# Optimization experiments

Hardware: AMD Instinct MI355X
Metric: run time of the kernel (lower is better)

Reference implementation:

```python
import jax, jax.numpy as jnp
import numpy as np

BETA = 0.95
THRESH = 1.0

def conv(x, w, b, stride):
    y = jax.lax.conv_general_dilated(x, w, (stride, stride), 'VALID',
                                     dimension_numbers=('NCHW', 'OIHW', 'NCHW'))
    return y + b[None, :, None, None]

def lif(mem, inp):
    # snntorch Leaky, reset_mechanism='subtract':
    # reset computed from previous mem, then mem = beta*mem + input - reset*thr, spk = H(mem - thr)
    reset = (mem > THRESH).astype(inp.dtype)
    mem = BETA * mem + inp - reset * THRESH
    spk = (mem > THRESH).astype(inp.dtype)
    return spk, mem

def setup_inputs() -> dict:
    key = jax.random.key(0)
    ks = jax.random.split(key, 7)
    B, T = 512, 4
    x = jax.random.uniform(ks[0], (B, T, 84, 84), jnp.float32) * 255.0  # raw pixel frames

    def init_conv(k, o, i, kh):
        lim = 1.0 / np.sqrt(i * kh * kh)
        k1, k2 = jax.random.split(k)
        return (jax.random.uniform(k1, (o, i, kh, kh), jnp.float32, -lim, lim),
                jax.random.uniform(k2, (o,), jnp.float32, -lim, lim))

    def init_lin(k, i, o):
        lim = 1.0 / np.sqrt(i)
        k1, k2 = jax.random.split(k)
        return (jax.random.uniform(k1, (o, i), jnp.float32, -lim, lim),
                jax.random.uniform(k2, (o,), jnp.float32, -lim, lim))

    w1, b1 = init_conv(ks[1], 32, 1, 8)
    w2, b2 = init_conv(ks[2], 64, 32, 4)
    w3, b3 = init_conv(ks[3], 64, 64, 3)
    wl, bl = init_lin(ks[4], 3136, 512)
    wh, bh = init_lin(ks[5], 512, 18)
    return {"x": x, "w1": w1, "b1": b1, "w2": w2, "b2": b2, "w3": w3, "b3": b3,
            "wl": wl, "bl": bl, "wh": wh, "bh": bh}

def reference(x, w1, b1, w2, b2, w3, b3, wl, bl, wh, bh):
    x = x / 255.0                                  # Plastic.forward scaling
    B, T = x.shape[0], x.shape[1]
    xt = jnp.transpose(x, (1, 0, 2, 3))[:, :, None]  # [T, B, 1, 84, 84]
    mem1 = jnp.zeros((B, 32, 20, 20), x.dtype)
    mem2 = jnp.zeros((B, 64, 9, 9), x.dtype)
    mem3 = jnp.zeros((B, 64, 7, 7), x.dtype)
    memf = jnp.zeros((B, 512), x.dtype)
    acc0 = jnp.zeros((B, 512), x.dtype)

    def step(carry, xs):
        mem1, mem2, mem3, memf, acc = carry
        o = conv(xs, w1, b1, 4)          # [B,32,20,20]
        s1, mem1 = lif(mem1, o)
        o = conv(s1, w2, b2, 2)          # [B,64,9,9]
        s2, mem2 = lif(mem2, o)
        o = conv(s2, w3, b3, 1)          # [B,64,7,7]
        s3, mem3 = lif(mem3, o)
        o = s3.reshape(B, -1) @ wl.T + bl  # [B,512]
        sf, memf = lif(memf, o)
        return (mem1, mem2, mem3, memf, acc + sf), None

    (mem1, mem2, mem3, memf, spk_out), _ = jax.lax.scan(
        step, (mem1, mem2, mem3, memf, acc0), xt)
    return (spk_out / T) @ wh.T + bh     # [B, 18]
```

## Files before the change

kernel.cpp:

```cpp
#include <hip/hip_runtime.h>

#define BETA 0.95f

__device__ __forceinline__ void lif_store(float inp, float* __restrict__ mem,
                                          float* __restrict__ spk, size_t idx, int t) {
    float m = t ? mem[idx] : 0.0f;
    float r = (m > 1.0f) ? 1.0f : 0.0f;
    m = BETA * m + inp - r;
    mem[idx] = m;
    spk[idx] = (m > 1.0f) ? 1.0f : 0.0f;
}

__global__ void transpose_w23(const float* __restrict__ w2, const float* __restrict__ w3,
                              float* __restrict__ w2t, float* __restrict__ w3t) {
    int i = blockIdx.x * 256 + threadIdx.x;
    if (i < 32768) { int oc = i >> 9;  int k = i & 511;      w2t[k * 64 + oc] = w2[i]; }
    if (i < 36864) { int oc = i / 576; int k = i - oc * 576; w3t[k * 64 + oc] = w3[i]; }
}

__global__ __launch_bounds__(320) void conv1_lif(const float* __restrict__ x,
        const float* __restrict__ w1, const float* __restrict__ b1,
        float* __restrict__ mem1, float* __restrict__ s1, int t)
{
    __shared__ float xs[7056];
    __shared__ __align__(16) float wt[2048];
    __shared__ float bs[32];
    const int b = blockIdx.x, tid = threadIdx.x;
    const float* xp = x + (size_t)(b * 4 + t) * 7056;
    for (int i = tid; i < 7056; i += 320) xs[i] = xp[i] * (1.0f / 255.0f);
    for (int i = tid; i < 2048; i += 320) { int oc = i >> 6, k = i & 63; wt[k * 32 + oc] = w1[i]; }
    if (tid < 32) bs[tid] = b1[tid];
    __syncthreads();

    const int ocg = tid & 7, row = tid >> 3;
    const int oc0 = ocg * 4;
    const int oy = row >> 1, ox0 = (row & 1) * 10;

    float acc[4][10];
    #pragma unroll
    for (int j = 0; j < 4; j++) {
        const float bv = bs[oc0 + j];
        #pragma unroll
        for (int i = 0; i < 10; i++) acc[j][i] = bv;
    }

    for (int ky = 0; ky < 8; ky++) {
        const float* xr = &xs[(oy * 4 + ky) * 84 + ox0 * 4];
        #pragma unroll
        for (int kx = 0; kx < 8; kx++) {
            const float4 w4 = *(const float4*)&wt[(ky * 8 + kx) * 32 + oc0];
            const float wv[4] = {w4.x, w4.y, w4.z, w4.w};
            float xv[10];
            #pragma unroll
            for (int i = 0; i < 10; i++) xv[i] = xr[kx + 4 * i];
            #pragma unroll
            for (int j = 0; j < 4; j++)
                #pragma unroll
                for (int i = 0; i < 10; i++)
                    acc[j][i] += wv[j] * xv[i];
        }
    }

    const size_t base = (size_t)b * 12800 + (size_t)oc0 * 400 + oy * 20 + ox0;
    #pragma unroll
    for (int j = 0; j < 4; j++)
        #pragma unroll
        for (int i = 0; i < 10; i++)
            lif_store(acc[j][i], mem1, s1, base + (size_t)j * 400 + i, t);
}

__global__ __launch_bounds__(448) void conv2_lif(const float* __restrict__ s1,
        const float* __restrict__ w2t, const float* __restrict__ b2,
        float* __restrict__ mem2, float* __restrict__ s2, int t)
{
    __shared__ float ins[12800];
    __shared__ __align__(16) float wt[64 * 64];
    __shared__ float bs[64];
    const int b = blockIdx.x, tid = threadIdx.x;
    const float* ip = s1 + (size_t)b * 12800;
    for (int i = tid; i < 12800; i += 448) ins[i] = ip[i];
    if (tid < 64) bs[tid] = b2[tid];

    const int ocg = tid & 15, pid = tid >> 4;
    const int oc0 = ocg * 4;
    const int oy = pid / 3, ox0 = (pid % 3) * 3;
    const bool act = (pid < 27);
    __syncthreads();

    float acc[4][3];
    #pragma unroll
    for (int j = 0; j < 4; j++) {
        const float bv = bs[oc0 + j];
        #pragma unroll
        for (int i = 0; i < 3; i++) acc[j][i] = bv;
    }

    for (int kc = 0; kc < 512; kc += 64) {
        for (int i = tid; i < 4096; i += 448) wt[i] = w2t[kc * 64 + i];
        __syncthreads();
        if (act) {
            const int ic0 = kc >> 4;
            #pragma unroll
            for (int icl = 0; icl < 4; icl++) {
                const float* inc = &ins[(ic0 + icl) * 400];
                #pragma unroll
                for (int ky = 0; ky < 4; ky++) {
                    const float* xr = &inc[(oy * 2 + ky) * 20 + ox0 * 2];
                    #pragma unroll
                    for (int kx = 0; kx < 4; kx++) {
                        const float4 w4 = *(const float4*)&wt[(icl * 16 + ky * 4 + kx) * 64 + oc0];
                        const float x0 = xr[kx], x1 = xr[kx + 2], x2 = xr[kx + 4];
                        acc[0][0] += w4.x * x0; acc[0][1] += w4.x * x1; acc[0][2] += w4.x * x2;
                        acc[1][0] += w4.y * x0; acc[1][1] += w4.y * x1; acc[1][2] += w4.y * x2;
                        acc[2][0] += w4.z * x0; acc[2][1] += w4.z * x1; acc[2][2] += w4.z * x2;
                        acc[3][0] += w4.w * x0; acc[3][1] += w4.w * x1; acc[3][2] += w4.w * x2;
                    }
                }
            }
        }
        __syncthreads();
    }

    if (act) {
        const size_t base = (size_t)b * 5184 + (size_t)oc0 * 81 + oy * 9 + ox0;
        #pragma unroll
        for (int j = 0; j < 4; j++)
            #pragma unroll
            for (int i = 0; i < 3; i++)
                lif_store(acc[j][i], mem2, s2, base + (size_t)j * 81 + i, t);
    }
}

__global__ __launch_bounds__(256) void conv3_lif(const float* __restrict__ s2,
        const float* __restrict__ w3t, const float* __restrict__ b3,
        float* __restrict__ mem3, float* __restrict__ s3, int t)
{
    __shared__ float ins[5184];
    __shared__ __align__(8) float wt[72 * 64];
    __shared__ float bs[64];
    const int b = blockIdx.x, tid = threadIdx.x;
    const float* ip = s2 + (size_t)b * 5184;
    for (int i = tid; i < 5184; i += 256) ins[i] = ip[i];
    if (tid < 64) bs[tid] = b3[tid];

    const int ocg = tid & 31, oy = tid >> 5;
    const int oc0 = ocg * 2;
    const bool act = (oy < 7);
    __syncthreads();

    float acc[2][7];
    #pragma unroll
    for (int j = 0; j < 2; j++) {
        const float bv = bs[oc0 + j];
        #pragma unroll
        for (int i = 0; i < 7; i++) acc[j][i] = bv;
    }

    for (int kc = 0; kc < 576; kc += 72) {
        for (int i = tid; i < 4608; i += 256) wt[i] = w3t[kc * 64 + i];
        __syncthreads();
        if (act) {
            const int ic0 = kc / 9;
            #pragma unroll
            for (int icl = 0; icl < 8; icl++) {
                const float* inc = &ins[(ic0 + icl) * 81];
                #pragma unroll
                for (int ky = 0; ky < 3; ky++) {
                    const float* xr = &inc[(oy + ky) * 9];
                    float xv[9];
                    #pragma unroll
                    for (int i = 0; i < 9; i++) xv[i] = xr[i];
                    #pragma unroll
                    for (int kx = 0; kx < 3; kx++) {
                        const float2 w2v = *(const float2*)&wt[(icl * 9 + ky * 3 + kx) * 64 + oc0];
                        #pragma unroll
                        for (int i = 0; i < 7; i++) {
                            acc[0][i] += w2v.x * xv[kx + i];
                            acc[1][i] += w2v.y * xv[kx + i];
                        }
                    }
                }
            }
        }
        __syncthreads();
    }

    if (act) {
        const size_t base = (size_t)b * 3136 + (size_t)oc0 * 49 + oy * 7;
        #pragma unroll
        for (int j = 0; j < 2; j++)
            #pragma unroll
            for (int i = 0; i < 7; i++)
                lif_store(acc[j][i], mem3, s3, base + (size_t)j * 49 + i, t);
    }
}

__global__ __launch_bounds__(256) void transpose_mk(const float* __restrict__ s3,
        const float* __restrict__ wl, float* __restrict__ s3t, float* __restrict__ wlt)
{
    __shared__ float T[64][65];
    const int c0 = blockIdx.x * 64;
    const int r0 = blockIdx.y * 64;
    const float* src = blockIdx.z ? wl : s3;
    float* dst = blockIdx.z ? wlt : s3t;
    const int tid = threadIdx.x;
    #pragma unroll
    for (int i = 0; i < 4; i++) {
        const int f = tid + 256 * i;
        const int r = f >> 4, cq = (f & 15) * 4;
        const float4 v = *(const float4*)&src[(size_t)(r0 + r) * 3136 + c0 + cq];
        T[r][cq + 0] = v.x; T[r][cq + 1] = v.y; T[r][cq + 2] = v.z; T[r][cq + 3] = v.w;
    }
    __syncthreads();
    #pragma unroll
    for (int i = 0; i < 4; i++) {
        const int f = tid + 256 * i;
        const int c = f >> 4, rq = (f & 15) * 4;
        float4 v;
        v.x = T[rq + 0][c]; v.y = T[rq + 1][c]; v.z = T[rq + 2][c]; v.w = T[rq + 3][c];
        *(float4*)&dst[(size_t)(c0 + c) * 512 + r0 + rq] = v;
    }
}

__global__ __launch_bounds__(256) void fc_gemm(const float* __restrict__ s3t,
        const float* __restrict__ wlt, float* __restrict__ part)
{
    __shared__ __align__(16) float As[64][68];
    __shared__ __align__(16) float Bs[64][68];
    const int bid = blockIdx.x;
    const int tile = bid & 63, split = bid >> 6;
    const int m0 = (tile & 7) * 64, n0 = (tile >> 3) * 64;
    const int tid = threadIdx.x;
    const int tn = (tid & 15) * 4, tm = (tid >> 4) * 4;
    float acc[4][4] = {};

    for (int sc = 0; sc < 7; sc++) {
        const int kc = split * 448 + sc * 64;
        __syncthreads();
        #pragma unroll
        for (int i = 0; i < 4; i++) {
            const int f = tid + 256 * i;
            const int k = f >> 4, mq = (f & 15) * 4;
            *(float4*)&As[k][mq] = *(const float4*)&s3t[(size_t)(kc + k) * 512 + m0 + mq];
            *(float4*)&Bs[k][mq] = *(const float4*)&wlt[(size_t)(kc + k) * 512 + n0 + mq];
        }
        __syncthreads();
        #pragma unroll 8
        for (int k = 0; k < 64; k++) {
            const float4 a = *(const float4*)&As[k][tm];
            const float4 b = *(const float4*)&Bs[k][tn];
            acc[0][0] += a.x * b.x; acc[0][1] += a.x * b.y; acc[0][2] += a.x * b.z; acc[0][3] += a.x * b.w;
            acc[1][0] += a.y * b.x; acc[1][1] += a.y * b.y; acc[1][2] += a.y * b.z; acc[1][3] += a.y * b.w;
            acc[2][0] += a.z * b.x; acc[2][1] += a.z * b.y; acc[2][2] += a.z * b.z; acc[2][3] += a.z * b.w;
            acc[3][0] += a.w * b.x; acc[3][1] += a.w * b.y; acc[3][2] += a.w * b.z; acc[3][3] += a.w * b.w;
        }
    }

    #pragma unroll
    for (int r = 0; r < 4; r++) {
        float4 v; v.x = acc[r][0]; v.y = acc[r][1]; v.z = acc[r][2]; v.w = acc[r][3];
        *(float4*)&part[(size_t)split * 262144 + (size_t)(m0 + tm + r) * 512 + n0 + tn] = v;
    }
}

__global__ __launch_bounds__(256) void fc_reduce_lif(const float* __restrict__ part,
        const float* __restrict__ bl, float* __restrict__ memf,
        float* __restrict__ accum, int t)
{
    const int gid = blockIdx.x * 256 + threadIdx.x;
    const int n = gid & 511;
    float s = part[gid];
    #pragma unroll
    for (int sp = 1; sp < 7; sp++) s += part[(size_t)sp * 262144 + gid];
    s += bl[n];
    const float mp = t ? memf[gid] : 0.0f;
    const float r = (mp > 1.0f) ? 1.0f : 0.0f;
    const float mnew = BETA * mp + s - r;
    memf[gid] = mnew;
    const float spk = (mnew > 1.0f) ? 1.0f : 0.0f;
    accum[gid] = (t ? accum[gid] : 0.0f) + spk;
}

__global__ void head_k(const float* __restrict__ accum, const float* __restrict__ wh,
                       const float* __restrict__ bh, float* __restrict__ out)
{
    const int gid = blockIdx.x * 256 + threadIdx.x;
    if (gid >= 512 * 18) return;
    const int b = gid / 18, o = gid - b * 18;
    const float* av = accum + (size_t)b * 512;
    const float* wv = wh + (size_t)o * 512;
    float s = bh[o];
    for (int k = 0; k < 512; k++) s += (av[k] * 0.25f) * wv[k];
    out[gid] = s;
}

extern "C" void kernel_launch(void* const* d_in, const int* in_sizes, int n_in,
                              void* d_out, int out_size, void* d_ws, size_t ws_size,
                              hipStream_t stream)
{
    const float* x  = (const float*)d_in[0];
    const float* w1 = (const float*)d_in[1];
    const float* b1 = (const float*)d_in[2];
    const float* w2 = (const float*)d_in[3];
    const float* b2 = (const float*)d_in[4];
    const float* w3 = (const float*)d_in[5];
    const float* b3 = (const float*)d_in[6];
    const float* wl = (const float*)d_in[7];
    const float* bl = (const float*)d_in[8];
    const float* wh = (const float*)d_in[9];
    const float* bh = (const float*)d_in[10];

    float* ws   = (float*)d_ws;
    float* mem1 = ws;
    float* mem2 = mem1 + 6553600;
    float* mem3 = mem2 + 2654208;
    float* memf = mem3 + 1605632;
    float* acc  = memf + 262144;
    float* s1   = acc  + 262144;
    float* s2   = s1 + 6553600;
    float* s3   = s2 + 2654208;
    float* w2t  = s3 + 1605632;
    float* w3t  = w2t + 32768;

    float* s3t_buf = s1;
    float* wlt_buf = s1 + 1605632;
    float* part    = s1 + 3211264;

    transpose_w23<<<144, 256, 0, stream>>>(w2, w3, w2t, w3t);

    for (int t = 0; t < 4; t++) {
        conv1_lif<<<512, 320, 0, stream>>>(x, w1, b1, mem1, s1, t);
        conv2_lif<<<512, 448, 0, stream>>>(s1, w2t, b2, mem2, s2, t);
        conv3_lif<<<512, 256, 0, stream>>>(s2, w3t, b3, mem3, s3, t);
        transpose_mk<<<dim3(49, 8, 2), 256, 0, stream>>>(s3, wl, s3t_buf, wlt_buf);
        fc_gemm<<<448, 256, 0, stream>>>(s3t_buf, wlt_buf, part);
        fc_reduce_lif<<<1024, 256, 0, stream>>>(part, bl, memf, acc, t);
    }
    head_k<<<36, 256, 0, stream>>>(acc, wh, bh, (float*)d_out);
}
```

Baseline: 1.107 ms.

## Retile conv2 so each thread computes a full output row for four channels

conv2 now uses 192 threads where each active thread computes 4 output channels by 9 output columns, in place of 4 by 3, and loads the input row as float4 vectors into registers. Input and weight staging into shared memory use float4 copies, and the barrier is moved to the top of the chunk loop. The aim is more reuse of each weight and input load per FMA and fewer idle threads. It raises register pressure (36 accumulators plus a 20-float row) and gives 48 of 192 threads nothing to compute, which may reduce occupancy.

```diff
diff --git a/kernel.cpp b/kernel.cpp
--- a/kernel.cpp
+++ b/kernel.cpp
@@ -69,35 +69,45 @@
             lif_store(acc[j][i], mem1, s1, base + (size_t)j * 400 + i, t);
 }
 
-__global__ __launch_bounds__(448) void conv2_lif(const float* __restrict__ s1,
+__global__ __launch_bounds__(192) void conv2_lif(const float* __restrict__ s1,
         const float* __restrict__ w2t, const float* __restrict__ b2,
         float* __restrict__ mem2, float* __restrict__ s2, int t)
 {
-    __shared__ float ins[12800];
-    __shared__ __align__(16) float wt[64 * 64];
+    __shared__ __align__(16) float ins[12800];
+    __shared__ __align__(16) float wt[4096];
     __shared__ float bs[64];
     const int b = blockIdx.x, tid = threadIdx.x;
     const float* ip = s1 + (size_t)b * 12800;
-    for (int i = tid; i < 12800; i += 448) ins[i] = ip[i];
+    for (int i = tid; i < 3200; i += 192)
+        *(float4*)&ins[i * 4] = *(const float4*)&ip[i * 4];
     if (tid < 64) bs[tid] = b2[tid];
 
-    const int ocg = tid & 15, pid = tid >> 4;
+    const int ocg = tid & 15, row = tid >> 4;
     const int oc0 = ocg * 4;
-    const int oy = pid / 3, ox0 = (pid % 3) * 3;
-    const bool act = (pid < 27);
-    __syncthreads();
-
-    float acc[4][3];
+    const bool act = (row < 9);
+
+    float acc[4][9];
     #pragma unroll
     for (int j = 0; j < 4; j++) {
         const float bv = bs[oc0 + j];
-        #pragma unroll
-        for (int i = 0; i < 3; i++) acc[j][i] = bv;
-    }
-
+        (void)bv;
+    }
+
+    bool inited = false;
     for (int kc = 0; kc < 512; kc += 64) {
-        for (int i = tid; i < 4096; i += 448) wt[i] = w2t[kc * 64 + i];
-        __syncthreads();
+        __syncthreads();
+        for (int i = tid; i < 1024; i += 192)
+            *(float4*)&wt[i * 4] = *(const float4*)&w2t[(size_t)kc * 64 + i * 4];
+        __syncthreads();
+        if (!inited) {
+            #pragma unroll
+            for (int j = 0; j < 4; j++) {
+                const float bv = bs[oc0 + j];
+                #pragma unroll
+                for (int i = 0; i < 9; i++) acc[j][i] = bv;
+            }
+            inited = true;
+        }
         if (act) {
             const int ic0 = kc >> 4;
             #pragma unroll
@@ -105,28 +115,37 @@
                 const float* inc = &ins[(ic0 + icl) * 400];
                 #pragma unroll
                 for (int ky = 0; ky < 4; ky++) {
-                    const float* xr = &inc[(oy * 2 + ky) * 20 + ox0 * 2];
+                    const float* xr = &inc[(2 * row + ky) * 20];
+                    float xv[20];
+                    #pragma unroll
+                    for (int q = 0; q < 5; q++) {
+                        const float4 v = *(const float4*)&xr[q * 4];
+                        xv[q * 4 + 0] = v.x; xv[q * 4 + 1] = v.y;
+                        xv[q * 4 + 2] = v.z; xv[q * 4 + 3] = v.w;
+                    }
                     #pragma unroll
                     for (int kx = 0; kx < 4; kx++) {
                         const float4 w4 = *(const float4*)&wt[(icl * 16 + ky * 4 + kx) * 64 + oc0];
-                        const float x0 = xr[kx], x1 = xr[kx + 2], x2 = xr[kx + 4];
-                        acc[0][0] += w4.x * x0; acc[0][1] += w4.x * x1; acc[0][2] += w4.x * x2;
-                        acc[1][0] += w4.y * x0; acc[1][1] += w4.y * x1; acc[1][2] += w4.y * x2;
-                        acc[2][0] += w4.z * x0; acc[2][1] += w4.z * x1; acc[2][2] += w4.z * x2;
-                        acc[3][0] += w4.w * x0; acc[3][1] += w4.w * x1; acc[3][2] += w4.w * x2;
+                        #pragma unroll
+                        for (int i = 0; i < 9; i++) {
+                            const float xvv = xv[kx + 2 * i];
+                            acc[0][i] += w4.x * xvv;
+                            acc[1][i] += w4.y * xvv;
+                            acc[2][i] += w4.z * xvv;
+                            acc[3][i] += w4.w * xvv;
+                        }
                     }
                 }
             }
         }
-        __syncthreads();
     }
 
     if (act) {
-        const size_t base = (size_t)b * 5184 + (size_t)oc0 * 81 + oy * 9 + ox0;
+        const size_t base = (size_t)b * 5184 + (size_t)oc0 * 81 + (size_t)row * 9;
         #pragma unroll
         for (int j = 0; j < 4; j++)
             #pragma unroll
-            for (int i = 0; i < 3; i++)
+            for (int i = 0; i < 9; i++)
                 lif_store(acc[j][i], mem2, s2, base + (size_t)j * 81 + i, t);
     }
 }
@@ -330,7 +349,7 @@
 
     for (int t = 0; t < 4; t++) {
         conv1_lif<<<512, 320, 0, stream>>>(x, w1, b1, mem1, s1, t);
-        conv2_lif<<<512, 448, 0, stream>>>(s1, w2t, b2, mem2, s2, t);
+        conv2_lif<<<512, 192, 0, stream>>>(s1, w2t, b2, mem2, s2, t);
         conv3_lif<<<512, 256, 0, stream>>>(s2, w3t, b3, mem3, s3, t);
         transpose_mk<<<dim3(49, 8, 2), 256, 0, stream>>>(s3, wl, s3t_buf, wlt_buf);
         fc_gemm<<<448, 256, 0, stream>>>(s3t_buf, wlt_buf, part);
```

New measurement: 1.189 ms. +7.4%, slower.
